# Optimization experiments

Measured on AMD Instinct MI355X. Metric: run time of the kernel, lower is better.

Reference implementation:

```python
import jax, jax.numpy as jnp
import numpy as np

EMBED_DIM = 1024
NUM_HEADS = 16
HEAD_DIM = EMBED_DIM // NUM_HEADS
BZ, Q_LEN, CACHE_LEN = 4, 512, 1536


def setup_inputs() -> dict:
    key = jax.random.key(0)
    ks = jax.random.split(key, 8)
    inp = {
        "hidden_states": jax.random.normal(ks[0], (BZ, Q_LEN, EMBED_DIM), jnp.float32),
        "attention_mask": jnp.zeros((BZ, 1, 1, CACHE_LEN + Q_LEN), jnp.float32),
        "k_cache": jax.random.normal(ks[1], (BZ, CACHE_LEN, EMBED_DIM), jnp.float32),
        "v_cache": jax.random.normal(ks[2], (BZ, CACHE_LEN, EMBED_DIM), jnp.float32),
        "Wq": jax.random.normal(ks[3], (EMBED_DIM, EMBED_DIM), jnp.float32) * 0.02,
        "bq": jnp.zeros((EMBED_DIM,), jnp.float32),
        "Wk": jax.random.normal(ks[4], (EMBED_DIM, EMBED_DIM), jnp.float32) * 0.02,
        "bk": jnp.zeros((EMBED_DIM,), jnp.float32),
        "Wv": jax.random.normal(ks[5], (EMBED_DIM, EMBED_DIM), jnp.float32) * 0.02,
        "bv": jnp.zeros((EMBED_DIM,), jnp.float32),
        "Wo": jax.random.normal(ks[6], (EMBED_DIM, EMBED_DIM), jnp.float32) * 0.02,
        "bo": jnp.zeros((EMBED_DIM,), jnp.float32),
    }
    return inp


def reference(hidden_states, attention_mask, k_cache, v_cache,
              Wq, bq, Wk, bk, Wv, bv, Wo, bo):
    bz, q_len, embed_dim = hidden_states.shape
    # projections (nn.Linear: x @ W.T + b)
    q = hidden_states @ Wq.T + bq
    k_new = hidden_states @ Wk.T + bk
    v_new = hidden_states @ Wv.T + bv
    # KV-cache concat (self_attn path)
    k = jnp.concatenate([k_cache, k_new], axis=1)  # [bz, kv_len, E]
    v = jnp.concatenate([v_cache, v_new], axis=1)
    q_begin = k_cache.shape[1]
    kv_len = k.shape[1]
    # split heads -> [bz, H, L, D]
    qh = q.reshape(bz, q_len, NUM_HEADS, HEAD_DIM).transpose(0, 2, 1, 3)
    kh = k.reshape(bz, kv_len, NUM_HEADS, HEAD_DIM).transpose(0, 2, 1, 3)
    vh = v.reshape(bz, kv_len, NUM_HEADS, HEAD_DIM).transpose(0, 2, 1, 3)
    scores = jnp.einsum("bhqd,bhkd->bhqk", qh, kh) / (HEAD_DIM ** 0.5)
    # causal mask slice causal_mask[q_begin:q_begin+q_len, :kv_len]
    rows = q_begin + jnp.arange(q_len)          # absolute query positions
    cols = jnp.arange(kv_len)
    causal = jnp.where(cols[None, :] > rows[:, None], -jnp.inf, 0.0).astype(scores.dtype)
    scores = scores + attention_mask + causal
    probs = jax.nn.softmax(scores, axis=-1)
    ctx = jnp.einsum("bhqk,bhkd->bhqd", probs, vh)
    ctx = ctx.transpose(0, 2, 1, 3).reshape(bz, q_len, embed_dim)
    out = ctx @ Wo.T + bo
    return out, k, v
```

## Files before the change

### kernel.cpp

```cpp
#include <hip/hip_runtime.h>
#include <hip/hip_bf16.h>
#include <stdint.h>

#define BZv 4
#define QL 512
#define CL 1536
#define KVL 2048
#define EMB 1024
#define NH 16
#define HD 64
#define QSCALE 0.18033688011112042f
#define NG 2048

typedef __attribute__((ext_vector_type(8))) short short8;
typedef __attribute__((ext_vector_type(4))) float floatx4;

__device__ __forceinline__ unsigned short f2b(float f) {
  union { float f; unsigned int u; } v; v.f = f;
  return (unsigned short)((v.u + 0x7FFFu + ((v.u >> 16) & 1u)) >> 16);
}

__device__ __forceinline__ ushort2 pk2(float a, float b) {
  union { __hip_bfloat162 h; ushort2 u; } c;
  c.h = __float22bfloat162_rn(make_float2(a, b));
  return c.u;
}

#if __has_builtin(__builtin_amdgcn_exp2f)
#define EXP2F(x) __builtin_amdgcn_exp2f(x)
#else
#define EXP2F(x) exp2f(x)
#endif

__device__ __forceinline__ void gload_lds16(const void* g, void* l) {
  __builtin_amdgcn_global_load_lds(
      (const __attribute__((address_space(1))) unsigned char*)g,
      (__attribute__((address_space(3))) unsigned char*)l, 16, 0, 0);
}

__global__ __launch_bounds__(256) void prep_kernel(
    const float* __restrict__ hid, const float* __restrict__ Wq, const float* __restrict__ Wk,
    const float* __restrict__ Wv, const float* __restrict__ Wo,
    const float* __restrict__ kc, const float* __restrict__ vc, const float* __restrict__ msk,
    unsigned short* __restrict__ Xb, unsigned short* __restrict__ Wqb, unsigned short* __restrict__ Wkb,
    unsigned short* __restrict__ Wvb, unsigned short* __restrict__ Wob,
    unsigned short* __restrict__ Kb, unsigned short* __restrict__ Vb,
    float* __restrict__ kf, float* __restrict__ vf, unsigned short* __restrict__ wb)
{
  const long HID4 = (long)BZv * QL * EMB / 4;
  const long W4   = (long)EMB * EMB / 4;
  const long C4   = (long)BZv * CL * EMB / 4;
  const long t0 = HID4, t1 = t0 + W4, t2 = t1 + W4, t3 = t2 + W4, t4 = t3 + W4;
  const long t5 = t4 + C4, t6 = t5 + C4;
  const long total = t6 + (long)BZv * KVL / 4;
  for (long i = (long)blockIdx.x * blockDim.x + threadIdx.x; i < total;
       i += (long)gridDim.x * blockDim.x) {
    if (i < t4) {
      const float* src; unsigned short* dst; long j;
      if (i < t0)      { src = hid; dst = Xb;  j = i; }
      else if (i < t1) { src = Wq;  dst = Wqb; j = i - t0; }
      else if (i < t2) { src = Wk;  dst = Wkb; j = i - t1; }
      else if (i < t3) { src = Wv;  dst = Wvb; j = i - t2; }
      else             { src = Wo;  dst = Wob; j = i - t3; }
      float4 v = ((const float4*)src)[j];
      ushort4 o; o.x = f2b(v.x); o.y = f2b(v.y); o.z = f2b(v.z); o.w = f2b(v.w);
      ((ushort4*)dst)[j] = o;
    } else if (i < t6) {
      bool isV = (i >= t5);
      long j = i - (isV ? t5 : t4);
      const float* src = isV ? vc : kc;
      float4 v = ((const float4*)src)[j];
      long e4 = j * 4;
      int b = (int)(e4 / ((long)CL * EMB));
      long rem = e4 - (long)b * CL * EMB;
      long doff = (long)b * KVL * EMB + rem;
      if (isV) {
        *((float4*)(vf + doff)) = v;
        int row = (int)(rem >> 10);
        float w = __expf(msk[b * KVL + row]);
        ushort4 o; o.x = f2b(v.x * w); o.y = f2b(v.y * w);
        o.z = f2b(v.z * w); o.w = f2b(v.w * w);
        *((ushort4*)(Vb + doff)) = o;
      } else {
        *((float4*)(kf + doff)) = v;
        ushort4 o; o.x = f2b(v.x); o.y = f2b(v.y); o.z = f2b(v.z); o.w = f2b(v.w);
        *((ushort4*)(Kb + doff)) = o;
      }
    } else {
      long j = i - t6;
      float4 m4 = ((const float4*)msk)[j];
      ushort4 o;
      o.x = f2b(__expf(m4.x)); o.y = f2b(__expf(m4.y));
      o.z = f2b(__expf(m4.z)); o.w = f2b(__expf(m4.w));
      ((ushort4*)wb)[j] = o;
    }
  }
}

__global__ __launch_bounds__(256) void qkv_gemm(
    const unsigned short* __restrict__ Xb,
    const unsigned short* __restrict__ Wqb, const unsigned short* __restrict__ Wkb,
    const unsigned short* __restrict__ Wvb,
    const float* __restrict__ bq, const float* __restrict__ bk, const float* __restrict__ bv,
    const float* __restrict__ msk,
    unsigned short* __restrict__ Qb, unsigned short* __restrict__ Kb, unsigned short* __restrict__ Vb,
    float* __restrict__ kf, float* __restrict__ vf)
{
  __shared__ unsigned short At[128 * 32];
  __shared__ unsigned short Bt[64 * 32];
  const int tid = threadIdx.x, lane = tid & 63, wave = tid >> 6;
  const int quad = lane >> 4, l = lane & 15;
  const int mat = blockIdx.x >> 4;
  const int ncol = (blockIdx.x & 15) * 64;
  const int mbase = blockIdx.y * 128;
  const unsigned short* W = (mat == 0) ? Wqb : (mat == 1) ? Wkb : Wvb;
  const float* bias = (mat == 0) ? bq : (mat == 1) ? bk : bv;
  const int srow = tid >> 2, slds = tid & 3;
  const int rh = wave * 32;

  floatx4 zero = {0.f, 0.f, 0.f, 0.f};
  floatx4 acc[2][4];
#pragma unroll
  for (int i = 0; i < 2; i++)
#pragma unroll
    for (int j = 0; j < 4; j++) acc[i][j] = zero;

  for (int k0 = 0; k0 < EMB; k0 += 32) {
    __syncthreads();
#pragma unroll
    for (int s = 0; s < 2; s++) {
      int row = s * 64 + srow;
      int gc = slds ^ (row & 3);
      gload_lds16(Xb + (size_t)(mbase + row) * EMB + k0 + gc * 8, &At[row * 32 + slds * 8]);
    }
    {
      int row = srow;
      int gc = slds ^ (row & 3);
      gload_lds16(W + (size_t)(ncol + row) * EMB + k0 + gc * 8, &Bt[row * 32 + slds * 8]);
    }
    __syncthreads();
    short8 af[2], bfr[4];
#pragma unroll
    for (int rt = 0; rt < 2; rt++) {
      int row = rh + rt * 16 + l;
      af[rt] = *(const short8*)&At[row * 32 + ((quad ^ (row & 3)) * 8)];
    }
#pragma unroll
    for (int ct = 0; ct < 4; ct++) {
      int row = ct * 16 + l;
      bfr[ct] = *(const short8*)&Bt[row * 32 + ((quad ^ (row & 3)) * 8)];
    }
#pragma unroll
    for (int rt = 0; rt < 2; rt++)
#pragma unroll
      for (int ct = 0; ct < 4; ct++)
        acc[rt][ct] = __builtin_amdgcn_mfma_f32_16x16x32_bf16(af[rt], bfr[ct], acc[rt][ct], 0, 0, 0);
  }

#pragma unroll
  for (int ct = 0; ct < 4; ct++) {
    int col = ncol + ct * 16 + l;
    float bb = bias[col];
#pragma unroll
    for (int rt = 0; rt < 2; rt++)
#pragma unroll
      for (int r = 0; r < 4; r++) {
        int m = mbase + rh + rt * 16 + quad * 4 + r;
        float val = acc[rt][ct][r] + bb;
        if (mat == 0) {
          Qb[(size_t)m * EMB + col] = f2b(val * QSCALE);
        } else {
          size_t a = ((size_t)(m >> 9) * KVL + CL + (m & 511)) * EMB + col;
          if (mat == 1) { Kb[a] = f2b(val); kf[a] = val; }
          else {
            float w = __expf(msk[(m >> 9) * KVL + CL + (m & 511)]);
            Vb[a] = f2b(val * w); vf[a] = val;
          }
        }
      }
  }
}

__global__ __launch_bounds__(256) void oproj_gemm(
    const unsigned short* __restrict__ A, const unsigned short* __restrict__ W,
    const float* __restrict__ bias, float* __restrict__ out)
{
  __shared__ unsigned short At[64 * 32];
  __shared__ unsigned short Bt[64 * 32];
  const int tid = threadIdx.x, lane = tid & 63, wave = tid >> 6;
  const int quad = lane >> 4, l = lane & 15;
  const int ncol = blockIdx.x * 64;
  const int mbase = blockIdx.y * 64;
  const int srow = tid >> 2, slds = tid & 3;
  const int rh = (wave & 1) * 32, ch = (wave >> 1) * 32;

  floatx4 zero = {0.f, 0.f, 0.f, 0.f};
  floatx4 acc[2][2];
#pragma unroll
  for (int i = 0; i < 2; i++)
#pragma unroll
    for (int j = 0; j < 2; j++) acc[i][j] = zero;

  for (int k0 = 0; k0 < EMB; k0 += 32) {
    __syncthreads();
    {
      int gc = slds ^ (srow & 3);
      gload_lds16(A + (size_t)(mbase + srow) * EMB + k0 + gc * 8, &At[srow * 32 + slds * 8]);
      gload_lds16(W + (size_t)(ncol + srow) * EMB + k0 + gc * 8, &Bt[srow * 32 + slds * 8]);
    }
    __syncthreads();
    short8 af[2], bfr[2];
#pragma unroll
    for (int rt = 0; rt < 2; rt++) {
      int row = rh + rt * 16 + l;
      af[rt] = *(const short8*)&At[row * 32 + ((quad ^ (row & 3)) * 8)];
    }
#pragma unroll
    for (int ct = 0; ct < 2; ct++) {
      int row = ch + ct * 16 + l;
      bfr[ct] = *(const short8*)&Bt[row * 32 + ((quad ^ (row & 3)) * 8)];
    }
#pragma unroll
    for (int rt = 0; rt < 2; rt++)
#pragma unroll
      for (int ct = 0; ct < 2; ct++)
        acc[rt][ct] = __builtin_amdgcn_mfma_f32_16x16x32_bf16(af[rt], bfr[ct], acc[rt][ct], 0, 0, 0);
  }

#pragma unroll
  for (int ct = 0; ct < 2; ct++) {
    int col = ncol + ch + ct * 16 + l;
    float bb = bias[col];
#pragma unroll
    for (int rt = 0; rt < 2; rt++)
#pragma unroll
      for (int r = 0; r < 4; r++) {
        int m = mbase + rh + rt * 16 + quad * 4 + r;
        out[(size_t)m * EMB + col] = acc[rt][ct][r] + bb;
      }
  }
}

__global__ __launch_bounds__(256, 4) void attn_kernel(
    const unsigned short* __restrict__ Qb, const unsigned short* __restrict__ Kb,
    const unsigned short* __restrict__ Vb, const unsigned short* __restrict__ wb,
    float* __restrict__ PO, float* __restrict__ PM, float* __restrict__ PD)
{
  __shared__ unsigned short Kt[2][64 * 64];
  __shared__ unsigned short Vt[65 * 72];
  __shared__ unsigned short Pl[4][16 * 72];

  const int bid = blockIdx.x;
  const int seg = bid >> 9;
  const int id = bid & 511;
  const int hb = id & 63, qt = id >> 6;
  const int b = hb >> 4, h = hb & 15;
  const int tid = threadIdx.x, lane = tid & 63, wave = tid >> 6;
  const int quad = lane >> 4, l = lane & 15;
  const int qbase = qt * 64 + wave * 16;

  const int nt_tot = (CL >> 6) + qt + 1;
  const int n0 = nt_tot >> 1;
  const int t_beg = seg ? n0 : 0;
  const int t_end = seg ? nt_tot : n0;

  const unsigned short* qp = Qb + (size_t)(b * QL + qbase + l) * EMB + h * HD + quad * 8;
  const short8 bq0 = *(const short8*)qp;
  const short8 bq1 = *(const short8*)(qp + 32);

  floatx4 zero = {0.f, 0.f, 0.f, 0.f};
  floatx4 o[4], o4 = zero;
#pragma unroll
  for (int c = 0; c < 4; c++) o[c] = zero;
  float mr = -INFINITY;

  const int vp = tid & 31, vg = tid >> 5;
  const unsigned short* vsrc = Vb + (size_t)(b * KVL) * EMB + h * HD + vg * 8;
  const unsigned short* wsrc = wb + (size_t)b * KVL + 2 * vp;
  const unsigned short* ksrc = Kb + (size_t)(b * KVL) * EMB + h * HD;
  const int sw = l & 7;

  uint4 va, vbr; ushort2 wn;
  auto VLOAD = [&](int t) {
    const unsigned short* vs = vsrc + (size_t)(t * 64 + 2 * vp) * EMB;
    va = *(const uint4*)vs;
    vbr = *(const uint4*)(vs + EMB);
    if (vg == 0) wn = *(const ushort2*)(wsrc + t * 64);
  };
  auto VSTAGE = [&]() {
    const unsigned short* pa = (const unsigned short*)&va;
    const unsigned short* pb = (const unsigned short*)&vbr;
#pragma unroll
    for (int j = 0; j < 8; j++) {
      ushort2 tt; tt.x = pa[j]; tt.y = pb[j];
      *(ushort2*)&Vt[(vg * 8 + j) * 72 + 2 * vp] = tt;
    }
    if (vg == 0) *(ushort2*)&Vt[64 * 72 + 2 * vp] = wn;
  };
  auto GLOAD_K = [&](int t, int buf) {
    const int kv0 = t * 64;
#pragma unroll
    for (int s = 0; s < 2; s++) {
      int g = s * 256 + tid;
      int r = g >> 3, k = g & 7;
      gload_lds16(ksrc + (size_t)(kv0 + r) * EMB + ((k ^ (r & 7)) * 8),
                  &Kt[buf][g * 8]);
    }
  };

  VLOAD(t_beg);
  GLOAD_K(t_beg, 0);
  __syncthreads();
  VSTAGE();
  if (t_beg + 1 < t_end) VLOAD(t_beg + 1);
  __syncthreads();

  int cur = 0;
  for (int t = t_beg; t < t_end; ++t) {
    if (t + 1 < t_end) GLOAD_K(t + 1, cur ^ 1);
    const int kv0 = t * 64;
    floatx4 s[4];
#pragma unroll
    for (int c = 0; c < 4; c++) {
      const int rr = c * 16 + l;
      const unsigned short* krow = &Kt[cur][rr * 64];
      short8 k0 = *(const short8*)&krow[(quad ^ sw) * 8];
      short8 k1 = *(const short8*)&krow[((quad + 4) ^ sw) * 8];
      s[c] = __builtin_amdgcn_mfma_f32_16x16x32_bf16(k0, bq0, zero, 0, 0, 0);
      s[c] = __builtin_amdgcn_mfma_f32_16x16x32_bf16(k1, bq1, s[c], 0, 0, 0);
    }
    if (kv0 + 63 > CL + qbase) {
      const int lim = CL + qbase + l;
#pragma unroll
      for (int c = 0; c < 4; c++) {
        int kvb = kv0 + c * 16 + quad * 4;
#pragma unroll
        for (int r = 0; r < 4; r++)
          s[c][r] = (kvb + r <= lim) ? s[c][r] : -INFINITY;
      }
    }
    float u0 = fmaxf(fmaxf(s[0][0], s[0][1]), fmaxf(s[0][2], s[0][3]));
    float u1 = fmaxf(fmaxf(s[1][0], s[1][1]), fmaxf(s[1][2], s[1][3]));
    float u2 = fmaxf(fmaxf(s[2][0], s[2][1]), fmaxf(s[2][2], s[2][3]));
    float u3 = fmaxf(fmaxf(s[3][0], s[3][1]), fmaxf(s[3][2], s[3][3]));
    float lmax = fmaxf(fmaxf(u0, u1), fmaxf(u2, u3));
    lmax = fmaxf(lmax, __shfl_xor(lmax, 16, 64));
    lmax = fmaxf(lmax, __shfl_xor(lmax, 32, 64));
    float mnew = fmaxf(mr, lmax);
    float alpha = EXP2F(mr - mnew);
    mr = mnew;
#pragma unroll
    for (int c = 0; c < 4; c++) {
      float p0 = EXP2F(s[c][0] - mnew), p1 = EXP2F(s[c][1] - mnew);
      float p2 = EXP2F(s[c][2] - mnew), p3 = EXP2F(s[c][3] - mnew);
      ushort2 lo = pk2(p0, p1), hi = pk2(p2, p3);
      ushort4 pk; pk.x = lo.x; pk.y = lo.y; pk.z = hi.x; pk.w = hi.y;
      *(ushort4*)&Pl[wave][l * 72 + c * 16 + quad * 4] = pk;
    }
#pragma unroll
    for (int c = 0; c < 4; c++)
#pragma unroll
      for (int r = 0; r < 4; r++) o[c][r] *= alpha;
#pragma unroll
    for (int r = 0; r < 4; r++) o4[r] *= alpha;
    asm volatile("s_waitcnt lgkmcnt(0)" ::: "memory");
    short8 pf0 = *(const short8*)&Pl[wave][l * 72 + quad * 8];
    short8 pf1 = *(const short8*)&Pl[wave][l * 72 + 32 + quad * 8];
    short8 vw0 = *(const short8*)&Vt[64 * 72 + quad * 8];
    short8 vw1 = *(const short8*)&Vt[64 * 72 + 32 + quad * 8];
    o4 = __builtin_amdgcn_mfma_f32_16x16x32_bf16(vw0, pf0, o4, 0, 0, 0);
    o4 = __builtin_amdgcn_mfma_f32_16x16x32_bf16(vw1, pf1, o4, 0, 0, 0);
#pragma unroll
    for (int c = 0; c < 4; c++) {
      short8 a0v = *(const short8*)&Vt[(c * 16 + l) * 72 + quad * 8];
      short8 a1v = *(const short8*)&Vt[(c * 16 + l) * 72 + 32 + quad * 8];
      o[c] = __builtin_amdgcn_mfma_f32_16x16x32_bf16(a0v, pf0, o[c], 0, 0, 0);
      o[c] = __builtin_amdgcn_mfma_f32_16x16x32_bf16(a1v, pf1, o[c], 0, 0, 0);
    }
    __syncthreads();
    if (t + 1 < t_end) {
      VSTAGE();
      if (t + 2 < t_end) VLOAD(t + 2);
    }
    __syncthreads();
    cur ^= 1;
  }

  const int gid = hb * 32 + qt * 4 + wave;
  float* po = PO + ((size_t)(seg * NG + gid)) * 1024 + l * 64;
#pragma unroll
  for (int c = 0; c < 4; c++)
    *(floatx4*)&po[c * 16 + quad * 4] = o[c];
  if (quad == 0) {
    PM[(size_t)(seg * NG + gid) * 16 + l] = mr;
    PD[(size_t)(seg * NG + gid) * 16 + l] = o4[0];
  }
}

__global__ __launch_bounds__(256) void attn_combine(
    const float* __restrict__ PO, const float* __restrict__ PM, const float* __restrict__ PD,
    unsigned short* __restrict__ Cb)
{
  const int tid = threadIdx.x, wave = tid >> 6, lane = tid & 63;
  const int quad = lane >> 4, l = lane & 15;
  const int gid = blockIdx.x * 4 + wave;
  const int hb = gid >> 5, qt = (gid >> 2) & 7, wv = gid & 3;
  const int b = hb >> 4, h = hb & 15;
  const int q = qt * 64 + wv * 16 + l;

  float m0 = PM[(size_t)gid * 16 + l];
  float m1 = PM[(size_t)(NG + gid) * 16 + l];
  float d0 = PD[(size_t)gid * 16 + l];
  float d1 = PD[(size_t)(NG + gid) * 16 + l];
  float M = fmaxf(m0, m1);
  float a0 = EXP2F(m0 - M), a1 = EXP2F(m1 - M);
  float inv = 1.0f / (d0 * a0 + d1 * a1);
  a0 *= inv; a1 *= inv;

  const float* p0 = PO + (size_t)gid * 1024 + l * 64 + quad * 16;
  const float* p1 = p0 + (size_t)NG * 1024;
  unsigned short* cp = Cb + (size_t)(b * QL + q) * EMB + h * HD + quad * 16;
#pragma unroll
  for (int v = 0; v < 4; v++) {
    float4 x0 = *(const float4*)(p0 + v * 4);
    float4 x1 = *(const float4*)(p1 + v * 4);
    ushort4 w4;
    w4.x = f2b(x0.x * a0 + x1.x * a1);
    w4.y = f2b(x0.y * a0 + x1.y * a1);
    w4.z = f2b(x0.z * a0 + x1.z * a1);
    w4.w = f2b(x0.w * a0 + x1.w * a1);
    *(ushort4*)(cp + v * 4) = w4;
  }
}

extern "C" void kernel_launch(void* const* d_in, const int* in_sizes, int n_in,
                              void* d_out, int out_size, void* d_ws, size_t ws_size,
                              hipStream_t stream) {
  const float* hid  = (const float*)d_in[0];
  const float* mask = (const float*)d_in[1];
  const float* kc   = (const float*)d_in[2];
  const float* vc   = (const float*)d_in[3];
  const float* Wq   = (const float*)d_in[4];
  const float* bq   = (const float*)d_in[5];
  const float* Wk   = (const float*)d_in[6];
  const float* bk   = (const float*)d_in[7];
  const float* Wv   = (const float*)d_in[8];
  const float* bv   = (const float*)d_in[9];
  const float* Wo   = (const float*)d_in[10];
  const float* bo   = (const float*)d_in[11];

  float* out_f = (float*)d_out;
  float* kf = out_f + (size_t)BZv * QL * EMB;
  float* vf = kf + (size_t)BZv * KVL * EMB;

  char* p = (char*)d_ws;
  unsigned short* Xb  = (unsigned short*)p; p += (size_t)BZv * QL * EMB * 2;
  unsigned short* Wqb = (unsigned short*)p; p += (size_t)EMB * EMB * 2;
  unsigned short* Wkb = (unsigned short*)p; p += (size_t)EMB * EMB * 2;
  unsigned short* Wvb = (unsigned short*)p; p += (size_t)EMB * EMB * 2;
  unsigned short* Wob = (unsigned short*)p; p += (size_t)EMB * EMB * 2;
  unsigned short* Qb  = (unsigned short*)p; p += (size_t)BZv * QL * EMB * 2;
  unsigned short* Kb  = (unsigned short*)p; p += (size_t)BZv * KVL * EMB * 2;
  unsigned short* Vb  = (unsigned short*)p; p += (size_t)BZv * KVL * EMB * 2;
  unsigned short* Cb  = (unsigned short*)p; p += (size_t)BZv * QL * EMB * 2;
  unsigned short* wbp = (unsigned short*)p; p += (size_t)BZv * KVL * 2;
  float* POp = (float*)p; p += (size_t)2 * NG * 1024 * 4;
  float* PMp = (float*)p; p += (size_t)2 * NG * 16 * 4;
  float* PDp = (float*)p; p += (size_t)2 * NG * 16 * 4;

  prep_kernel<<<2048, 256, 0, stream>>>(hid, Wq, Wk, Wv, Wo, kc, vc, mask,
                                        Xb, Wqb, Wkb, Wvb, Wob, Kb, Vb, kf, vf, wbp);
  qkv_gemm<<<dim3(48, 16), 256, 0, stream>>>(Xb, Wqb, Wkb, Wvb, bq, bk, bv, mask,
                                             Qb, Kb, Vb, kf, vf);
  attn_kernel<<<1024, 256, 0, stream>>>(Qb, Kb, Vb, wbp, POp, PMp, PDp);
  attn_combine<<<512, 256, 0, stream>>>(POp, PMp, PDp, Cb);
  oproj_gemm<<<dim3(16, 32), 256, 0, stream>>>(Cb, Wob, bo, out_f);
}
```

Baseline: 248.7 us.

## Fuse split-KV combine into attention via atomic counters; restructure prep with nontemporal stores

```diff
diff --git a/kernel.cpp b/kernel.cpp
--- a/kernel.cpp
+++ b/kernel.cpp
@@ -14,6 +14,7 @@
 
 typedef __attribute__((ext_vector_type(8))) short short8;
 typedef __attribute__((ext_vector_type(4))) float floatx4;
+typedef __attribute__((ext_vector_type(4))) float fx4;
 
 __device__ __forceinline__ unsigned short f2b(float f) {
   union { float f; unsigned int u; } v; v.f = f;
@@ -24,6 +25,19 @@
   union { __hip_bfloat162 h; ushort2 u; } c;
   c.h = __float22bfloat162_rn(make_float2(a, b));
   return c.u;
+}
+
+__device__ __forceinline__ ushort4 cvt4(fx4 v) {
+  ushort4 o; o.x = f2b(v.x); o.y = f2b(v.y); o.z = f2b(v.z); o.w = f2b(v.w);
+  return o;
+}
+__device__ __forceinline__ ushort4 cvt4w(fx4 v, float w) {
+  ushort4 o; o.x = f2b(v.x * w); o.y = f2b(v.y * w);
+  o.z = f2b(v.z * w); o.w = f2b(v.w * w);
+  return o;
+}
+__device__ __forceinline__ void nts(fx4* p, fx4 v) {
+  __builtin_nontemporal_store(v, p);
 }
 
 #if __has_builtin(__builtin_amdgcn_exp2f)
@@ -45,55 +59,63 @@
     unsigned short* __restrict__ Xb, unsigned short* __restrict__ Wqb, unsigned short* __restrict__ Wkb,
     unsigned short* __restrict__ Wvb, unsigned short* __restrict__ Wob,
     unsigned short* __restrict__ Kb, unsigned short* __restrict__ Vb,
-    float* __restrict__ kf, float* __restrict__ vf, unsigned short* __restrict__ wb)
+    float* __restrict__ kf, float* __restrict__ vf, unsigned short* __restrict__ wb,
+    int* __restrict__ flags)
 {
-  const long HID4 = (long)BZv * QL * EMB / 4;
-  const long W4   = (long)EMB * EMB / 4;
-  const long C4   = (long)BZv * CL * EMB / 4;
-  const long t0 = HID4, t1 = t0 + W4, t2 = t1 + W4, t3 = t2 + W4, t4 = t3 + W4;
-  const long t5 = t4 + C4, t6 = t5 + C4;
-  const long total = t6 + (long)BZv * KVL / 4;
-  for (long i = (long)blockIdx.x * blockDim.x + threadIdx.x; i < total;
-       i += (long)gridDim.x * blockDim.x) {
-    if (i < t4) {
-      const float* src; unsigned short* dst; long j;
-      if (i < t0)      { src = hid; dst = Xb;  j = i; }
-      else if (i < t1) { src = Wq;  dst = Wqb; j = i - t0; }
-      else if (i < t2) { src = Wk;  dst = Wkb; j = i - t1; }
-      else if (i < t3) { src = Wv;  dst = Wvb; j = i - t2; }
-      else             { src = Wo;  dst = Wob; j = i - t3; }
-      float4 v = ((const float4*)src)[j];
-      ushort4 o; o.x = f2b(v.x); o.y = f2b(v.y); o.z = f2b(v.z); o.w = f2b(v.w);
-      ((ushort4*)dst)[j] = o;
-    } else if (i < t6) {
-      bool isV = (i >= t5);
-      long j = i - (isV ? t5 : t4);
-      const float* src = isV ? vc : kc;
-      float4 v = ((const float4*)src)[j];
-      long e4 = j * 4;
-      int b = (int)(e4 / ((long)CL * EMB));
-      long rem = e4 - (long)b * CL * EMB;
-      long doff = (long)b * KVL * EMB + rem;
+  const int blk = blockIdx.x, tid = threadIdx.x;
+  if (blk < 768) {
+    const float* src; unsigned short* dst; int base;
+    if (blk < 256) { src = hid; dst = Xb; base = blk * 2048; }
+    else {
+      int w = (blk - 256) >> 7, wo = (blk - 256) & 127;
+      src = (w == 0) ? Wq : (w == 1) ? Wk : (w == 2) ? Wv : Wo;
+      dst = (w == 0) ? Wqb : (w == 1) ? Wkb : (w == 2) ? Wvb : Wob;
+      base = wo * 2048;
+    }
+    const fx4* s4 = (const fx4*)src;
+    ushort4* d4 = (ushort4*)dst;
+#pragma unroll
+    for (int it = 0; it < 4; ++it) {
+      int u = base + it * 512 + tid * 2;
+      fx4 a = s4[u], b = s4[u + 1];
+      d4[u] = cvt4(a); d4[u + 1] = cvt4(b);
+    }
+  } else if (blk < 1792) {
+    const bool isV = blk >= 1280;
+    const int r = blk - (isV ? 1280 : 768);
+    const int bb = r >> 7, ko = r & 127;
+    const fx4* s4 = (const fx4*)((isV ? vc : kc) + (long)bb * CL * EMB);
+    fx4* f4 = (fx4*)((isV ? vf : kf) + (long)bb * KVL * EMB);
+    ushort4* b4 = (ushort4*)((isV ? Vb : Kb) + (long)bb * KVL * EMB);
+    const float* mrow = msk + bb * KVL;
+#pragma unroll
+    for (int it = 0; it < 6; ++it) {
+      int u = ko * 3072 + it * 512 + tid * 2;
+      fx4 a = s4[u], b = s4[u + 1];
+      nts(&f4[u], a); nts(&f4[u + 1], b);
       if (isV) {
-        *((float4*)(vf + doff)) = v;
-        int row = (int)(rem >> 10);
-        float w = __expf(msk[b * KVL + row]);
-        ushort4 o; o.x = f2b(v.x * w); o.y = f2b(v.y * w);
-        o.z = f2b(v.z * w); o.w = f2b(v.w * w);
-        *((ushort4*)(Vb + doff)) = o;
+        float w0 = __expf(mrow[u >> 8]);
+        float w1 = __expf(mrow[(u + 1) >> 8]);
+        b4[u] = cvt4w(a, w0); b4[u + 1] = cvt4w(b, w1);
       } else {
-        *((float4*)(kf + doff)) = v;
-        ushort4 o; o.x = f2b(v.x); o.y = f2b(v.y); o.z = f2b(v.z); o.w = f2b(v.w);
-        *((ushort4*)(Kb + doff)) = o;
+        b4[u] = cvt4(a); b4[u + 1] = cvt4(b);
       }
-    } else {
-      long j = i - t6;
-      float4 m4 = ((const float4*)msk)[j];
-      ushort4 o;
-      o.x = f2b(__expf(m4.x)); o.y = f2b(__expf(m4.y));
-      o.z = f2b(__expf(m4.z)); o.w = f2b(__expf(m4.w));
-      ((ushort4*)wb)[j] = o;
-    }
+    }
+  } else {
+    const fx4* m4 = (const fx4*)msk;
+    ushort4* w4 = (ushort4*)wb;
+#pragma unroll
+    for (int it = 0; it < 4; ++it) {
+      int u = it * 512 + tid * 2;
+      fx4 a = m4[u], b = m4[u + 1];
+      ushort4 oa, ob;
+      oa.x = f2b(__expf(a.x)); oa.y = f2b(__expf(a.y));
+      oa.z = f2b(__expf(a.z)); oa.w = f2b(__expf(a.w));
+      ob.x = f2b(__expf(b.x)); ob.y = f2b(__expf(b.y));
+      ob.z = f2b(__expf(b.z)); ob.w = f2b(__expf(b.w));
+      w4[u] = oa; w4[u + 1] = ob;
+    }
+    flags[tid] = 0; flags[tid + 256] = 0;
   }
 }
 
@@ -244,11 +266,13 @@
 __global__ __launch_bounds__(256, 4) void attn_kernel(
     const unsigned short* __restrict__ Qb, const unsigned short* __restrict__ Kb,
     const unsigned short* __restrict__ Vb, const unsigned short* __restrict__ wb,
-    float* __restrict__ PO, float* __restrict__ PM, float* __restrict__ PD)
+    float* __restrict__ PO, float* __restrict__ PM, float* __restrict__ PD,
+    int* __restrict__ flags, unsigned short* __restrict__ Cb)
 {
   __shared__ unsigned short Kt[2][64 * 64];
   __shared__ unsigned short Vt[65 * 72];
   __shared__ unsigned short Pl[4][16 * 72];
+  __shared__ int oldv;
 
   const int bid = blockIdx.x;
   const int seg = bid >> 9;
@@ -395,41 +419,32 @@
     PM[(size_t)(seg * NG + gid) * 16 + l] = mr;
     PD[(size_t)(seg * NG + gid) * 16 + l] = o4[0];
   }
-}
-
-__global__ __launch_bounds__(256) void attn_combine(
-    const float* __restrict__ PO, const float* __restrict__ PM, const float* __restrict__ PD,
-    unsigned short* __restrict__ Cb)
-{
-  const int tid = threadIdx.x, wave = tid >> 6, lane = tid & 63;
-  const int quad = lane >> 4, l = lane & 15;
-  const int gid = blockIdx.x * 4 + wave;
-  const int hb = gid >> 5, qt = (gid >> 2) & 7, wv = gid & 3;
-  const int b = hb >> 4, h = hb & 15;
-  const int q = qt * 64 + wv * 16 + l;
-
-  float m0 = PM[(size_t)gid * 16 + l];
-  float m1 = PM[(size_t)(NG + gid) * 16 + l];
-  float d0 = PD[(size_t)gid * 16 + l];
-  float d1 = PD[(size_t)(NG + gid) * 16 + l];
-  float M = fmaxf(m0, m1);
-  float a0 = EXP2F(m0 - M), a1 = EXP2F(m1 - M);
-  float inv = 1.0f / (d0 * a0 + d1 * a1);
-  a0 *= inv; a1 *= inv;
-
-  const float* p0 = PO + (size_t)gid * 1024 + l * 64 + quad * 16;
-  const float* p1 = p0 + (size_t)NG * 1024;
-  unsigned short* cp = Cb + (size_t)(b * QL + q) * EMB + h * HD + quad * 16;
-#pragma unroll
-  for (int v = 0; v < 4; v++) {
-    float4 x0 = *(const float4*)(p0 + v * 4);
-    float4 x1 = *(const float4*)(p1 + v * 4);
-    ushort4 w4;
-    w4.x = f2b(x0.x * a0 + x1.x * a1);
-    w4.y = f2b(x0.y * a0 + x1.y * a1);
-    w4.z = f2b(x0.z * a0 + x1.z * a1);
-    w4.w = f2b(x0.w * a0 + x1.w * a1);
-    *(ushort4*)(cp + v * 4) = w4;
+  __threadfence();
+  __syncthreads();
+  if (tid == 0) oldv = atomicAdd(&flags[id], 1);
+  __syncthreads();
+  if (oldv == 1) {
+    __threadfence();
+    const int oseg = seg ^ 1;
+    float m1 = PM[(size_t)(oseg * NG + gid) * 16 + l];
+    float d1 = PD[(size_t)(oseg * NG + gid) * 16 + l];
+    float m0 = mr, d0 = o4[0];
+    float M = fmaxf(m0, m1);
+    float a0 = EXP2F(m0 - M), a1 = EXP2F(m1 - M);
+    float inv = 1.0f / (d0 * a0 + d1 * a1);
+    a0 *= inv; a1 *= inv;
+    const fx4* po1 = (const fx4*)(PO + ((size_t)(oseg * NG + gid)) * 1024 + l * 64);
+    unsigned short* cp = Cb + (size_t)(b * QL + qbase + l) * EMB + h * HD;
+#pragma unroll
+    for (int c = 0; c < 4; c++) {
+      fx4 x1 = po1[c * 4 + quad];
+      ushort4 st;
+      st.x = f2b(o[c][0] * a0 + x1.x * a1);
+      st.y = f2b(o[c][1] * a0 + x1.y * a1);
+      st.z = f2b(o[c][2] * a0 + x1.z * a1);
+      st.w = f2b(o[c][3] * a0 + x1.w * a1);
+      *(ushort4*)(cp + c * 16 + quad * 4) = st;
+    }
   }
 }
 
@@ -467,12 +482,12 @@
   float* POp = (float*)p; p += (size_t)2 * NG * 1024 * 4;
   float* PMp = (float*)p; p += (size_t)2 * NG * 16 * 4;
   float* PDp = (float*)p; p += (size_t)2 * NG * 16 * 4;
-
-  prep_kernel<<<2048, 256, 0, stream>>>(hid, Wq, Wk, Wv, Wo, kc, vc, mask,
-                                        Xb, Wqb, Wkb, Wvb, Wob, Kb, Vb, kf, vf, wbp);
+  int* flg  = (int*)p;   p += 512 * 4;
+
+  prep_kernel<<<1793, 256, 0, stream>>>(hid, Wq, Wk, Wv, Wo, kc, vc, mask,
+                                        Xb, Wqb, Wkb, Wvb, Wob, Kb, Vb, kf, vf, wbp, flg);
   qkv_gemm<<<dim3(48, 16), 256, 0, stream>>>(Xb, Wqb, Wkb, Wvb, bq, bk, bv, mask,
                                              Qb, Kb, Vb, kf, vf);
-  attn_kernel<<<1024, 256, 0, stream>>>(Qb, Kb, Vb, wbp, POp, PMp, PDp);
-  attn_combine<<<512, 256, 0, stream>>>(POp, PMp, PDp, Cb);
+  attn_kernel<<<1024, 256, 0, stream>>>(Qb, Kb, Vb, wbp, POp, PMp, PDp, flg, Cb);
   oproj_gemm<<<dim3(16, 32), 256, 0, stream>>>(Cb, Wob, bo, out_f);
 }
```

Measured after the change: 419.1 us. +68.5%, slower.
